# Kernel optimization log

Measured on AMD Instinct MI355X. Metric: run time of the kernel, lower is better.

Reference implementation:

```python
import jax, jax.numpy as jnp
import numpy as np

NQ, NK, H, DH = 1024, 512, 8, 64


def setup_inputs() -> dict:
    key = jax.random.key(0)
    ks = jax.random.split(key, 8)
    b, n, d, g = 4, 4096, 1024, 4
    di = H * DH  # 512
    s = lambda fan: 1.0 / np.sqrt(fan)
    return {
        "x": jax.random.normal(ks[0], (b, n, d), jnp.float32),
        "w_qr": jax.random.normal(ks[1], (g, d), jnp.float32) * s(d),
        "w_kvr": jax.random.normal(ks[2], (g, d), jnp.float32) * s(d),
        "w_q": jax.random.normal(ks[3], (g, di, d), jnp.float32) * s(d),
        "w_kv": jax.random.normal(ks[4], (g, 2 * di, d), jnp.float32) * s(d),
        "w_out": jax.random.normal(ks[5], (g, d, di), jnp.float32) * s(di),
        "null_kv": jax.random.normal(ks[6], (2, g, H, 1, DH), jnp.float32),
        "null_token": jax.random.normal(ks[7], (1, 1, d), jnp.float32),
    }


def reference(x, w_qr, w_kvr, w_q, w_kv, w_out, null_kv, null_token):
    b, n, d = x.shape
    g = w_qr.shape[0]
    bidx = jnp.arange(b)[:, None, None]
    # --- routing: per-expert token scores, top-k select (router reference) ---
    q_logits = jnp.einsum("bnd,gd->bgn", x, w_qr)
    q_top, q_idx = jax.lax.top_k(q_logits, NQ)            # [b,g,NQ]
    q_scores = jax.nn.sigmoid(q_top)[..., None]           # [b,g,NQ,1]
    queries = x[bidx, q_idx]                              # [b,g,NQ,d]
    kv_logits = jnp.einsum("bnd,gd->bgn", x, w_kvr)
    kv_top, kv_idx = jax.lax.top_k(kv_logits, NK)
    kv_scores = jax.nn.sigmoid(kv_top)[:, :, None, :, None]  # [b,g,1,NK,1]
    key_values = x[bidx, kv_idx]                          # [b,g,NK,d]
    # --- grouped attention (1x1 grouped convs == per-group matmuls) ---
    q = jnp.einsum("bgnd,ged->bgne", queries, w_q)
    kv = jnp.einsum("bgnd,ged->bgne", key_values, w_kv)
    k, v = jnp.split(kv, 2, axis=-1)
    heads = lambda t: t.reshape(b, g, -1, H, DH).transpose(0, 1, 3, 2, 4)  # b g h n dh
    q, k, v = heads(q), heads(k), heads(v)
    v = v * kv_scores                                     # values_scale
    nk = jnp.broadcast_to(null_kv[0][None], (b, g, H, 1, DH))
    nv = jnp.broadcast_to(null_kv[1][None], (b, g, H, 1, DH))
    k = jnp.concatenate([nk, k], axis=-2)
    v = jnp.concatenate([nv, v], axis=-2)
    attn = jax.nn.softmax(jnp.einsum("bghid,bghjd->bghij", q, k) * DH ** -0.5, axis=-1)
    o = jnp.einsum("bghij,bghjd->bghid", attn, v)
    o = o.transpose(0, 1, 3, 2, 4).reshape(b, g, NQ, H * DH)
    o = jnp.einsum("bgne,gde->bgnd", o, w_out)
    o = o * q_scores
    # --- scatter-add back with count normalization ---
    flat_idx = q_idx.reshape(b, g * NQ)
    flat_o = o.reshape(b, g * NQ, d)
    b2 = jnp.arange(b)[:, None]
    summed = jnp.zeros_like(x).at[b2, flat_idx].add(flat_o)
    counts = jnp.zeros((b, n), x.dtype).at[b2, flat_idx].add(1.0)[..., None]
    meaned = summed / jnp.clip(counts, 1e-5)
    return jnp.where(counts > 0, meaned, null_token)
```

## Files before the change

### kernel.cpp

```cpp
#include <hip/hip_runtime.h>
#include <math.h>

#define NB 4
#define SEQ 4096
#define DM 1024
#define NG 4
#define DI 512
#define NQS 1024
#define NKS 512
#define NHD 8
#define DHD 64
#define VTS 520

typedef unsigned int u32;
typedef unsigned short u16;
typedef __bf16 bf16x8 __attribute__((ext_vector_type(8)));
typedef float f32x4 __attribute__((ext_vector_type(4)));

__device__ __forceinline__ float bf2f(u16 u) { return __uint_as_float(((u32)u) << 16); }
__device__ __forceinline__ u16 f2bf(float f) {
  u32 u = __float_as_uint(f);
  u32 r = (u + 0x7FFFu + ((u >> 16) & 1u)) >> 16;
  return (u16)r;
}
__device__ __forceinline__ u16 f2bfh(float f) {
  union { __bf16 b; u16 u; } cv;
  cv.b = (__bf16)f;
  return cv.u;
}

__global__ __launch_bounds__(256) void router_kernel(
    const float* __restrict__ x, const float* __restrict__ wqr,
    const float* __restrict__ wkvr, float* __restrict__ qlog,
    float* __restrict__ kvlog, u16* __restrict__ xbf) {
  int tid = threadIdx.x;
  int base = blockIdx.x * 8 + (tid >> 6) * 2;
  int lane = tid & 63;
  int b = base >> 12, tok = base & 4095;
  const float4* xr0 = (const float4*)(x + ((size_t)(b * SEQ + tok)) * DM);
  const float4* xr1 = xr0 + 256;
  float4 xv0[4], xv1[4];
#pragma unroll
  for (int i = 0; i < 4; i++) {
    xv0[i] = xr0[i * 64 + lane];
    xv1[i] = xr1[i * 64 + lane];
  }
  ushort4* xrow0 = (ushort4*)(xbf + ((size_t)(b * SEQ + tok)) * DM);
  ushort4* xrow1 = xrow0 + 256;
#pragma unroll
  for (int i = 0; i < 4; i++) {
    ushort4 o0, o1;
    o0.x = f2bf(xv0[i].x); o0.y = f2bf(xv0[i].y);
    o0.z = f2bf(xv0[i].z); o0.w = f2bf(xv0[i].w);
    o1.x = f2bf(xv1[i].x); o1.y = f2bf(xv1[i].y);
    o1.z = f2bf(xv1[i].z); o1.w = f2bf(xv1[i].w);
    xrow0[i * 64 + lane] = o0;
    xrow1[i * 64 + lane] = o1;
  }
  float a0[8], a1[8];
#pragma unroll
  for (int r = 0; r < 8; r++) {
    const float4* wr =
        (const float4*)(r < 4 ? wqr + (r << 10) : wkvr + ((r - 4) << 10));
    float s0 = 0.f, s1 = 0.f;
#pragma unroll
    for (int i = 0; i < 4; i++) {
      float4 w4 = wr[i * 64 + lane];
      s0 += xv0[i].x * w4.x + xv0[i].y * w4.y + xv0[i].z * w4.z + xv0[i].w * w4.w;
      s1 += xv1[i].x * w4.x + xv1[i].y * w4.y + xv1[i].z * w4.z + xv1[i].w * w4.w;
    }
    a0[r] = s0; a1[r] = s1;
  }
#pragma unroll
  for (int r = 0; r < 8; r++) {
#pragma unroll
    for (int off = 32; off >= 1; off >>= 1) {
      a0[r] += __shfl_xor(a0[r], off);
      a1[r] += __shfl_xor(a1[r], off);
    }
    if (lane == 0) {
      if (r < 4) {
        qlog[((b << 2) | r) * SEQ + tok] = a0[r];
        qlog[((b << 2) | r) * SEQ + tok + 1] = a1[r];
      } else {
        kvlog[((b << 2) | (r - 4)) * SEQ + tok] = a0[r];
        kvlog[((b << 2) | (r - 4)) * SEQ + tok + 1] = a1[r];
      }
    }
  }
}

__global__ __launch_bounds__(256) void topk_kernel(
    const float* __restrict__ qlog, const float* __restrict__ kvlog,
    int* __restrict__ qidx, float* __restrict__ qscore,
    int* __restrict__ kvidx, float* __restrict__ kvscore,
    int* __restrict__ qpos, const float* __restrict__ wq,
    const float* __restrict__ wkv, const float* __restrict__ wout,
    u16* __restrict__ wqbf, u16* __restrict__ wkvbf, u16* __restrict__ woutbf) {
  int tid = threadIdx.x;
  if (blockIdx.x >= 32) {
    int cid = blockIdx.x - 32;
#pragma unroll
    for (int j = 0; j < 4; j++) {
      int idx = cid * 1024 + j * 256 + tid;
      const float* src; u16* dst; int off;
      if (idx < 524288)        { src = wq;   dst = wqbf;   off = idx; }
      else if (idx < 1572864)  { src = wkv;  dst = wkvbf;  off = idx - 524288; }
      else                     { src = wout; dst = woutbf; off = idx - 1572864; }
      float4 v = ((const float4*)src)[off];
      ushort4 o;
      o.x = f2bf(v.x); o.y = f2bf(v.y); o.z = f2bf(v.z); o.w = f2bf(v.w);
      ((ushort4*)dst)[off] = o;
    }
    return;
  }
  __shared__ u32 keys[4096];
  __shared__ int eqlist[2048];
  __shared__ int scnt[4];
  __shared__ int s_gt, s_eq;
  int which = blockIdx.x >> 4;
  int bg = blockIdx.x & 15;
  int K = (which == 0) ? NQS : NKS;
  const float* L = ((which == 0) ? qlog : kvlog) + bg * 4096;
  int* out_idx = ((which == 0) ? qidx : kvidx) + bg * K;
  float* out_score = ((which == 0) ? qscore : kvscore) + bg * K;
  int* qposb = qpos + bg * 4096;
  for (int e = tid; e < 4096; e += 256) {
    u32 u = __float_as_uint(L[e]);
    keys[e] = (u >> 31) ? ~u : (u | 0x80000000u);
  }
  if (which == 0)
    for (int e = tid; e < 4096; e += 256) qposb[e] = -1;
  if (tid == 0) { s_gt = 0; s_eq = 0; }
  __syncthreads();
  u32 prefix = 0;
  int remaining = K;
  for (int bit = 31; bit >= 0; --bit) {
    u32 want = prefix | (1u << bit);
    u32 mask = ~((1u << bit) - 1u);
    int c = 0;
    for (int e = tid; e < 4096; e += 256) c += ((keys[e] & mask) == want) ? 1 : 0;
#pragma unroll
    for (int off = 32; off >= 1; off >>= 1) c += __shfl_xor(c, off);
    if ((tid & 63) == 0) scnt[tid >> 6] = c;
    __syncthreads();
    int total = scnt[0] + scnt[1] + scnt[2] + scnt[3];
    if (total >= remaining) prefix = want;
    else remaining -= total;
    __syncthreads();
  }
  u32 T = prefix;
  for (int e = tid; e < 4096; e += 256) {
    u32 k = keys[e];
    if (k > T) {
      int pos = atomicAdd(&s_gt, 1);
      out_idx[pos] = e;
      u32 uo = (k >> 31) ? (k & 0x7FFFFFFFu) : ~k;
      float v = __uint_as_float(uo);
      out_score[pos] = 1.0f / (1.0f + __expf(-v));
      if (which == 0) qposb[e] = pos;
    } else if (k == T) {
      int p = atomicAdd(&s_eq, 1);
      if (p < 2048) eqlist[p] = e;
    }
  }
  __syncthreads();
  int gt = s_gt;
  int eq = min(s_eq, 2048);
  int need = K - gt;
  for (int i = tid; i < eq; i += 256) {
    int my = eqlist[i];
    int rank = 0;
    for (int j = 0; j < eq; j++) rank += (eqlist[j] < my) ? 1 : 0;
    if (rank < need) {
      int pos = gt + rank;
      out_idx[pos] = my;
      u32 k2 = keys[my];
      u32 uo = (k2 >> 31) ? (k2 & 0x7FFFFFFFu) : ~k2;
      float v = __uint_as_float(uo);
      out_score[pos] = 1.0f / (1.0f + __expf(-v));
      if (which == 0) qposb[my] = pos;
    }
  }
}

struct Ptr4 { const u16* p[4]; };

__device__ __forceinline__ void mfma_core(Ptr4 A, Ptr4 B, u16* Asm, u16* Bsm,
                                          int ktiles, int tid, f32x4 (&acc)[4][4]) {
  int w = tid >> 6, lane = tid & 63;
  int col = lane & 15, quad = lane >> 4;
  int wr = w >> 1, wc = w & 1;
  for (int kt = 0; kt < ktiles; kt++) {
#pragma unroll
    for (int r = 0; r < 4; r++) {
      char* ldsA = (char*)Asm + (r * 256 + w * 64) * 16;
      __builtin_amdgcn_global_load_lds(
          (const __attribute__((address_space(1))) void*)(A.p[r] + kt * 64),
          (__attribute__((address_space(3))) void*)ldsA, 16, 0, 0);
    }
#pragma unroll
    for (int r = 0; r < 4; r++) {
      char* ldsB = (char*)Bsm + (r * 256 + w * 64) * 16;
      __builtin_amdgcn_global_load_lds(
          (const __attribute__((address_space(1))) void*)(B.p[r] + kt * 64),
          (__attribute__((address_space(3))) void*)ldsB, 16, 0, 0);
    }
    __syncthreads();
#pragma unroll
    for (int k04 = 0; k04 < 8; k04 += 4) {
      bf16x8 af[4], bfr[4];
#pragma unroll
      for (int t = 0; t < 4; t++) {
        int rowa = wr * 64 + t * 16 + col;
        int sp = (quad + k04) ^ (col & 7);
        af[t] = *(const bf16x8*)((const char*)Asm + (rowa * 8 + sp) * 16);
        int rowb = wc * 64 + t * 16 + col;
        bfr[t] = *(const bf16x8*)((const char*)Bsm + (rowb * 8 + sp) * 16);
      }
#pragma unroll
      for (int t = 0; t < 4; t++)
#pragma unroll
        for (int u = 0; u < 4; u++)
          acc[t][u] = __builtin_amdgcn_mfma_f32_16x16x32_bf16(af[t], bfr[u], acc[t][u], 0, 0, 0);
    }
    __syncthreads();
  }
}

__global__ __launch_bounds__(256) void gemm_qkvproj(
    const u16* __restrict__ xbf, const int* __restrict__ qidx,
    const int* __restrict__ kvidx, const u16* __restrict__ wqbf,
    const u16* __restrict__ wkvbf, const float* __restrict__ kvscore,
    u16* __restrict__ qbuf, u16* __restrict__ kbuf, u16* __restrict__ vtbuf) {
  __shared__ __align__(16) u16 Asm[8192], Bsm[8192];
  __shared__ int ridx[128];
  int tid = threadIdx.x;
  int id = blockIdx.x;
  bool is_q = (id & 1) == 0;
  int sid = id >> 1;
  int bg = sid >> 5, r5 = sid & 31;
  int b = bg >> 2, g = bg & 3;
  int w = tid >> 6, lane = tid & 63;
  int col = lane & 15, quad = lane >> 4;
  int wr = w >> 1, wc = w & 1;

  if (is_q) {
    int col0 = (r5 & 3) * 128, row0 = (r5 >> 2) * 128;
    if (tid < 128) ridx[tid] = qidx[bg * NQS + row0 + tid];
    __syncthreads();
    Ptr4 A, B;
#pragma unroll
    for (int r = 0; r < 4; r++) {
      int G = r * 256 + tid;
      int row = G >> 3;
      int seg = (G & 7) ^ (row & 7);
      A.p[r] = xbf + ((size_t)b * SEQ + ridx[row]) * DM + seg * 8;
      B.p[r] = wqbf + ((size_t)g * DI + col0 + row) * DM + seg * 8;
    }
    f32x4 acc[4][4] = {};
    mfma_core(A, B, Asm, Bsm, DM / 64, tid, acc);
#pragma unroll
    for (int t = 0; t < 4; t++)
#pragma unroll
      for (int u = 0; u < 4; u++)
#pragma unroll
        for (int r = 0; r < 4; r++) {
          int rowg = row0 + wr * 64 + t * 16 + quad * 4 + r;
          int colg = col0 + wc * 64 + u * 16 + col;
          qbuf[((size_t)bg * NQS + rowg) * DI + colg] = f2bf(acc[t][u][r] * 0.125f);
        }
  } else {
    int col0 = (r5 & 7) * 128, row0 = (r5 >> 3) * 128;
    if (tid < 128) ridx[tid] = kvidx[bg * NKS + row0 + tid];
    __syncthreads();
    Ptr4 A, B;
#pragma unroll
    for (int r = 0; r < 4; r++) {
      int G = r * 256 + tid;
      int row = G >> 3;
      int seg = (G & 7) ^ (row & 7);
      A.p[r] = xbf + ((size_t)b * SEQ + ridx[row]) * DM + seg * 8;
      B.p[r] = wkvbf + ((size_t)g * (2 * DI) + col0 + row) * DM + seg * 8;
    }
    f32x4 acc[4][4] = {};
    mfma_core(A, B, Asm, Bsm, DM / 64, tid, acc);
    if (col0 < DI) {
#pragma unroll
      for (int t = 0; t < 4; t++)
#pragma unroll
        for (int u = 0; u < 4; u++)
#pragma unroll
          for (int r = 0; r < 4; r++) {
            int rowg = row0 + wr * 64 + t * 16 + quad * 4 + r;
            int colg = col0 + wc * 64 + u * 16 + col;
            kbuf[((size_t)bg * NKS + rowg) * DI + colg] = f2bf(acc[t][u][r]);
          }
    } else {
#pragma unroll
      for (int t = 0; t < 4; t++) {
        int base = row0 + wr * 64 + t * 16 + quad * 4;
        float sc0 = kvscore[bg * NKS + base + 0];
        float sc1 = kvscore[bg * NKS + base + 1];
        float sc2 = kvscore[bg * NKS + base + 2];
        float sc3 = kvscore[bg * NKS + base + 3];
#pragma unroll
        for (int u = 0; u < 4; u++) {
          int vc = col0 - DI + wc * 64 + u * 16 + col;
          int h = vc >> 6, d = vc & 63;
          u32 lo = (u32)f2bf(acc[t][u][0] * sc0) | ((u32)f2bf(acc[t][u][1] * sc1) << 16);
          u32 hi = (u32)f2bf(acc[t][u][2] * sc2) | ((u32)f2bf(acc[t][u][3] * sc3) << 16);
          *(uint2*)&vtbuf[(((size_t)bg * NHD + h) * DHD + d) * VTS + base] =
              make_uint2(lo, hi);
        }
      }
    }
  }
}

__global__ __launch_bounds__(256) void gemm_outproj(
    const u16* __restrict__ obuf, const u16* __restrict__ woutbf,
    const float* __restrict__ qscore, float* __restrict__ oproj_lo,
    float* __restrict__ oproj_hi) {
  int bg = blockIdx.z, g = bg & 3;
  int row0 = blockIdx.y * 128, col0 = blockIdx.x * 128;
  __shared__ __align__(16) u16 Asm[8192], Bsm[8192];
  int tid = threadIdx.x;
  Ptr4 A, B;
#pragma unroll
  for (int r = 0; r < 4; r++) {
    int G = r * 256 + tid;
    int row = G >> 3;
    int seg = (G & 7) ^ (row & 7);
    A.p[r] = obuf + ((size_t)bg * NQS + row0 + row) * DI + seg * 8;
    B.p[r] = woutbf + ((size_t)g * DM + col0 + row) * DI + seg * 8;
  }
  f32x4 acc[4][4] = {};
  mfma_core(A, B, Asm, Bsm, DI / 64, tid, acc);
  int w = tid >> 6, lane = tid & 63;
  int col = lane & 15, quad = lane >> 4;
  int wr = w >> 1, wc = w & 1;
  float* obase = (bg < 8 ? oproj_lo : oproj_hi) + (size_t)(bg & 7) * NQS * DM;
#pragma unroll
  for (int t = 0; t < 4; t++)
#pragma unroll
    for (int r = 0; r < 4; r++) {
      int rowg = row0 + wr * 64 + t * 16 + quad * 4 + r;
      float sc = qscore[bg * NQS + rowg];
      float* orow = obase + (size_t)rowg * DM;
#pragma unroll
      for (int u = 0; u < 4; u++) {
        int colg = col0 + wc * 64 + u * 16 + col;
        orow[colg] = acc[t][u][r] * sc;
      }
    }
}

__global__ __launch_bounds__(256) void finalize_gather(
    const float* __restrict__ oproj_lo, const float* __restrict__ oproj_hi,
    const int* __restrict__ qpos, const float* __restrict__ null_token,
    float* __restrict__ dout) {
  int blk = blockIdx.x;
  int b = blk >> 12;
  int tok = blk & 4095;
  int tid = threadIdx.x;
  const float* obase = (b < 2) ? oproj_lo : oproj_hi;
  int zoff = (b & 1) * 4;
  float4 acc = {0.f, 0.f, 0.f, 0.f};
  int cnt = 0;
#pragma unroll
  for (int g = 0; g < 4; g++) {
    int pos = qpos[(((b << 2) | g)) * 4096 + tok];
    if (pos >= 0) {
      const float4* row =
          (const float4*)(obase + ((size_t)(zoff + g) * NQS + pos) * DM);
      float4 v = row[tid];
      acc.x += v.x; acc.y += v.y; acc.z += v.z; acc.w += v.w;
      cnt++;
    }
  }
  float4* dst = (float4*)(dout + ((size_t)b * SEQ + tok) * DM) + tid;
  if (cnt > 0) {
    float inv = 1.0f / cnt;
    acc.x *= inv; acc.y *= inv; acc.z *= inv; acc.w *= inv;
    *dst = acc;
  } else {
    *dst = ((const float4*)null_token)[tid];
  }
}

__global__ __launch_bounds__(256, 4) void attn_mfma(
    const u16* __restrict__ qbuf, const u16* __restrict__ kbuf,
    const u16* __restrict__ vtbuf, const float* __restrict__ null_kv,
    u16* __restrict__ obuf) {
  int qt = blockIdx.x;
  int h = blockIdx.y;
  int bg = blockIdx.z;
  int g = bg & 3;
  int tid = threadIdx.x;
  int w = tid >> 6, lane = tid & 63;
  int col = lane & 15, quad = lane >> 4;

  __shared__ __align__(16) u16 Ks[64][72];
  __shared__ __align__(16) u16 Vts[64][72];
  __shared__ __align__(16) u16 Ps[4][32][72];

  int q0 = qt * 128 + w * 32;
  const u16* qp0 = qbuf + ((size_t)bg * NQS + q0 + col) * DI + h * DHD + quad * 8;
  bf16x8 qa[2][2];
  qa[0][0] = *(const bf16x8*)qp0;
  qa[0][1] = *(const bf16x8*)(qp0 + 32);
  qa[1][0] = *(const bf16x8*)(qp0 + 16 * DI);
  qa[1][1] = *(const bf16x8*)(qp0 + 16 * DI + 32);

  const float* kn = null_kv + ((size_t)(0 * NG + g) * NHD + h) * DHD;
  const float* vn = null_kv + ((size_t)(1 * NG + g) * NHD + h) * DHD;
  float m_run[2], l_lane[2];
  f32x4 oacc[2][4];
#pragma unroll
  for (int s = 0; s < 2; s++) {
    float sn = 0.f;
#pragma unroll
    for (int i = 0; i < 8; i++) {
      sn += (float)qa[s][0][i] * kn[quad * 8 + i];
      sn += (float)qa[s][1][i] * kn[32 + quad * 8 + i];
    }
    sn += __shfl_xor(sn, 16);
    sn += __shfl_xor(sn, 32);
    m_run[s] = sn;
    l_lane[s] = (quad == 0) ? 1.f : 0.f;
  }
#pragma unroll
  for (int t = 0; t < 4; t++) {
    float v = vn[t * 16 + col];
    f32x4 tmp = {v, v, v, v};
    oacc[0][t] = tmp;
    oacc[1][t] = tmp;
  }

  int sr = tid >> 2, ss = tid & 3;
  const u16* kptr = kbuf + ((size_t)bg * NKS + sr) * DI + h * DHD + ss * 16;
  const u16* vptr = vtbuf + (((size_t)bg * NHD + h) * DHD + sr) * VTS + ss * 16;
  uint4* kdst = (uint4*)&Ks[sr][ss * 16];
  uint4* vdst = (uint4*)&Vts[sr][ss * 16];
  uint4 ck0, ck1, cv0, cv1;
  { const uint4* p = (const uint4*)kptr; ck0 = p[0]; ck1 = p[1]; }
  { const uint4* p = (const uint4*)vptr; cv0 = p[0]; cv1 = p[1]; }

  for (int c = 0; c < 8; ++c) {
    kdst[0] = ck0; kdst[1] = ck1;
    vdst[0] = cv0; vdst[1] = cv1;
    if (c < 7) {
      const uint4* p = (const uint4*)(kptr + (size_t)(c + 1) * 64 * DI);
      ck0 = p[0]; ck1 = p[1];
      const uint4* q4 = (const uint4*)(vptr + (c + 1) * 64);
      cv0 = q4[0]; cv1 = q4[1];
    }
    __syncthreads();

    f32x4 sv[2][4];
#pragma unroll
    for (int t = 0; t < 4; t++) {
      bf16x8 kb0 = *(const bf16x8*)&Ks[t * 16 + col][quad * 8];
      bf16x8 kb1 = *(const bf16x8*)&Ks[t * 16 + col][quad * 8 + 32];
      f32x4 z = {0.f, 0.f, 0.f, 0.f};
      f32x4 s0 = __builtin_amdgcn_mfma_f32_16x16x32_bf16(kb0, qa[0][0], z, 0, 0, 0);
      sv[0][t] = __builtin_amdgcn_mfma_f32_16x16x32_bf16(kb1, qa[0][1], s0, 0, 0, 0);
      f32x4 s1 = __builtin_amdgcn_mfma_f32_16x16x32_bf16(kb0, qa[1][0], z, 0, 0, 0);
      sv[1][t] = __builtin_amdgcn_mfma_f32_16x16x32_bf16(kb1, qa[1][1], s1, 0, 0, 0);
    }

#pragma unroll
    for (int s = 0; s < 2; s++) {
      float pm = sv[s][0][0];
#pragma unroll
      for (int t = 0; t < 4; t++)
#pragma unroll
        for (int r = 0; r < 4; r++) pm = fmaxf(pm, sv[s][t][r]);
      pm = fmaxf(pm, __shfl_xor(pm, 16));
      pm = fmaxf(pm, __shfl_xor(pm, 32));
      if (!__all(pm <= m_run[s] + 8.0f)) {
        float mnew = fmaxf(m_run[s], pm);
        float alpha = __expf(m_run[s] - mnew);
        m_run[s] = mnew;
        l_lane[s] *= alpha;
#pragma unroll
        for (int r = 0; r < 4; r++) {
          float a_o = __shfl(alpha, quad * 4 + r);
#pragma unroll
          for (int t = 0; t < 4; t++) oacc[s][t][r] *= a_o;
        }
      }
      float rs = 0.f;
#pragma unroll
      for (int t = 0; t < 4; t++) {
        float p0 = __expf(sv[s][t][0] - m_run[s]);
        float p1 = __expf(sv[s][t][1] - m_run[s]);
        float p2 = __expf(sv[s][t][2] - m_run[s]);
        float p3 = __expf(sv[s][t][3] - m_run[s]);
        rs += (p0 + p1) + (p2 + p3);
        u32 lo = (u32)f2bfh(p0) | ((u32)f2bfh(p1) << 16);
        u32 hi = (u32)f2bfh(p2) | ((u32)f2bfh(p3) << 16);
        *(uint2*)&Ps[w][s * 16 + col][t * 16 + quad * 4] = make_uint2(lo, hi);
      }
      l_lane[s] += rs;
    }

#pragma unroll
    for (int s2 = 0; s2 < 2; s2++) {
      bf16x8 pa0 = *(const bf16x8*)&Ps[w][col][s2 * 32 + quad * 8];
      bf16x8 pa1 = *(const bf16x8*)&Ps[w][16 + col][s2 * 32 + quad * 8];
#pragma unroll
      for (int t = 0; t < 4; t++) {
        bf16x8 vb = *(const bf16x8*)&Vts[t * 16 + col][s2 * 32 + quad * 8];
        oacc[0][t] = __builtin_amdgcn_mfma_f32_16x16x32_bf16(pa0, vb, oacc[0][t], 0, 0, 0);
        oacc[1][t] = __builtin_amdgcn_mfma_f32_16x16x32_bf16(pa1, vb, oacc[1][t], 0, 0, 0);
      }
    }
    __syncthreads();
  }

#pragma unroll
  for (int s = 0; s < 2; s++) {
    float l = l_lane[s];
    l += __shfl_xor(l, 16);
    l += __shfl_xor(l, 32);
    float inv = 1.0f / l;
#pragma unroll
    for (int r = 0; r < 4; r++) {
      float ir = __shfl(inv, quad * 4 + r);
#pragma unroll
      for (int t = 0; t < 4; t++) {
        obuf[((size_t)bg * NQS + q0 + s * 16 + quad * 4 + r) * DI + h * DHD +
             t * 16 + col] = f2bfh(oacc[s][t][r] * ir);
      }
    }
  }
}

extern "C" void kernel_launch(void* const* d_in, const int* in_sizes, int n_in,
                              void* d_out, int out_size, void* d_ws, size_t ws_size,
                              hipStream_t stream) {
  const float* x = (const float*)d_in[0];
  const float* wqr = (const float*)d_in[1];
  const float* wkvr = (const float*)d_in[2];
  const float* wq = (const float*)d_in[3];
  const float* wkv = (const float*)d_in[4];
  const float* wout = (const float*)d_in[5];
  const float* nullkv = (const float*)d_in[6];
  const float* nulltok = (const float*)d_in[7];
  float* out = (float*)d_out;
  char* ws = (char*)d_ws;
  float* qlog = (float*)(ws + 0);
  float* kvlog = (float*)(ws + 262144);
  int* qidx = (int*)(ws + 524288);
  int* kvidx = (int*)(ws + 589824);
  float* qscore = (float*)(ws + 622592);
  float* kvscore = (float*)(ws + 688128);
  u16* qbuf = (u16*)(ws + 786432);
  u16* kbuf = (u16*)(ws + 17563648);
  u16* vtbuf = (u16*)(ws + 25952256);
  u16* obuf = (u16*)(ws + 34476032);
  u16* xbf = (u16*)(ws + 51253248);
  u16* wqbf = (u16*)(ws + 84807680);
  u16* wkvbf = (u16*)(ws + 89001984);
  u16* woutbf = (u16*)(ws + 97390592);
  int* qpos = (int*)(ws + 0);
  float* oproj_lo = (float*)(ws + 786432);
  float* oproj_hi = (float*)(ws + 51253248);

  router_kernel<<<2048, 256, 0, stream>>>(x, wqr, wkvr, qlog, kvlog, xbf);
  topk_kernel<<<2080, 256, 0, stream>>>(qlog, kvlog, qidx, qscore, kvidx,
                                        kvscore, qpos, wq, wkv, wout, wqbf,
                                        wkvbf, woutbf);
  gemm_qkvproj<<<1024, 256, 0, stream>>>(xbf, qidx, kvidx, wqbf, wkvbf, kvscore,
                                         qbuf, kbuf, vtbuf);
  attn_mfma<<<dim3(8, 8, 16), 256, 0, stream>>>(qbuf, kbuf, vtbuf, nullkv, obuf);
  gemm_outproj<<<dim3(8, 8, 16), 256, 0, stream>>>(obuf, woutbf, qscore,
                                                   oproj_lo, oproj_hi);
  finalize_gather<<<16384, 256, 0, stream>>>(oproj_lo, oproj_hi, qpos, nulltok,
                                             out);
}
```

Measured before the change: 316.7 us.

## Store out-projection in bf16, shorten top-k radix passes, remap attention grid

The out-projection intermediate is now written as bf16 instead of fp32, and finalize_gather reads it back as bf16. This halves the bytes written and re-read between those two kernels, at the cost of rounding before the per-token averaging. The top-k radix select stops after 20 bits, which cuts the number of count passes. Remaining ties are then ranked by full key and index, so the selection stays exact as long as the tie list fits its buffer. The attention launch becomes a 1D grid whose block decode puts heads and batch-groups innermost, which changes the block scheduling order.

```diff
diff --git a/kernel.cpp b/kernel.cpp
--- a/kernel.cpp
+++ b/kernel.cpp
@@ -135,7 +135,7 @@
   __syncthreads();
   u32 prefix = 0;
   int remaining = K;
-  for (int bit = 31; bit >= 0; --bit) {
+  for (int bit = 31; bit >= 12; --bit) {
     u32 want = prefix | (1u << bit);
     u32 mask = ~((1u << bit) - 1u);
     int c = 0;
@@ -152,14 +152,15 @@
   u32 T = prefix;
   for (int e = tid; e < 4096; e += 256) {
     u32 k = keys[e];
-    if (k > T) {
+    u32 k20 = k & 0xFFFFF000u;
+    if (k20 > T) {
       int pos = atomicAdd(&s_gt, 1);
       out_idx[pos] = e;
       u32 uo = (k >> 31) ? (k & 0x7FFFFFFFu) : ~k;
       float v = __uint_as_float(uo);
       out_score[pos] = 1.0f / (1.0f + __expf(-v));
       if (which == 0) qposb[e] = pos;
-    } else if (k == T) {
+    } else if (k20 == T) {
       int p = atomicAdd(&s_eq, 1);
       if (p < 2048) eqlist[p] = e;
     }
@@ -170,13 +171,16 @@
   int need = K - gt;
   for (int i = tid; i < eq; i += 256) {
     int my = eqlist[i];
+    u32 myk = keys[my];
     int rank = 0;
-    for (int j = 0; j < eq; j++) rank += (eqlist[j] < my) ? 1 : 0;
+    for (int j = 0; j < eq; j++) {
+      u32 kj = keys[eqlist[j]];
+      rank += (kj > myk || (kj == myk && eqlist[j] < my)) ? 1 : 0;
+    }
     if (rank < need) {
       int pos = gt + rank;
       out_idx[pos] = my;
-      u32 k2 = keys[my];
-      u32 uo = (k2 >> 31) ? (k2 & 0x7FFFFFFFu) : ~k2;
+      u32 uo = (myk >> 31) ? (myk & 0x7FFFFFFFu) : ~myk;
       float v = __uint_as_float(uo);
       out_score[pos] = 1.0f / (1.0f + __expf(-v));
       if (which == 0) qposb[my] = pos;
@@ -320,8 +324,8 @@
 
 __global__ __launch_bounds__(256) void gemm_outproj(
     const u16* __restrict__ obuf, const u16* __restrict__ woutbf,
-    const float* __restrict__ qscore, float* __restrict__ oproj_lo,
-    float* __restrict__ oproj_hi) {
+    const float* __restrict__ qscore, u16* __restrict__ oproj_lo,
+    u16* __restrict__ oproj_hi) {
   int bg = blockIdx.z, g = bg & 3;
   int row0 = blockIdx.y * 128, col0 = blockIdx.x * 128;
   __shared__ __align__(16) u16 Asm[8192], Bsm[8192];
@@ -340,31 +344,31 @@
   int w = tid >> 6, lane = tid & 63;
   int col = lane & 15, quad = lane >> 4;
   int wr = w >> 1, wc = w & 1;
-  float* obase = (bg < 8 ? oproj_lo : oproj_hi) + (size_t)(bg & 7) * NQS * DM;
+  u16* obase = (bg < 8 ? oproj_lo : oproj_hi) + (size_t)(bg & 7) * NQS * DM;
 #pragma unroll
   for (int t = 0; t < 4; t++)
 #pragma unroll
     for (int r = 0; r < 4; r++) {
       int rowg = row0 + wr * 64 + t * 16 + quad * 4 + r;
       float sc = qscore[bg * NQS + rowg];
-      float* orow = obase + (size_t)rowg * DM;
+      u16* orow = obase + (size_t)rowg * DM;
 #pragma unroll
       for (int u = 0; u < 4; u++) {
         int colg = col0 + wc * 64 + u * 16 + col;
-        orow[colg] = acc[t][u][r] * sc;
+        orow[colg] = f2bfh(acc[t][u][r] * sc);
       }
     }
 }
 
 __global__ __launch_bounds__(256) void finalize_gather(
-    const float* __restrict__ oproj_lo, const float* __restrict__ oproj_hi,
+    const u16* __restrict__ oproj_lo, const u16* __restrict__ oproj_hi,
     const int* __restrict__ qpos, const float* __restrict__ null_token,
     float* __restrict__ dout) {
   int blk = blockIdx.x;
   int b = blk >> 12;
   int tok = blk & 4095;
   int tid = threadIdx.x;
-  const float* obase = (b < 2) ? oproj_lo : oproj_hi;
+  const u16* obase = (b < 2) ? oproj_lo : oproj_hi;
   int zoff = (b & 1) * 4;
   float4 acc = {0.f, 0.f, 0.f, 0.f};
   int cnt = 0;
@@ -372,10 +376,13 @@
   for (int g = 0; g < 4; g++) {
     int pos = qpos[(((b << 2) | g)) * 4096 + tok];
     if (pos >= 0) {
-      const float4* row =
-          (const float4*)(obase + ((size_t)(zoff + g) * NQS + pos) * DM);
-      float4 v = row[tid];
-      acc.x += v.x; acc.y += v.y; acc.z += v.z; acc.w += v.w;
+      const uint2* row =
+          (const uint2*)(obase + ((size_t)(zoff + g) * NQS + pos) * DM);
+      uint2 v = row[tid];
+      acc.x += bf2f((u16)(v.x & 0xFFFF));
+      acc.y += bf2f((u16)(v.x >> 16));
+      acc.z += bf2f((u16)(v.y & 0xFFFF));
+      acc.w += bf2f((u16)(v.y >> 16));
       cnt++;
     }
   }
@@ -393,9 +400,10 @@
     const u16* __restrict__ qbuf, const u16* __restrict__ kbuf,
     const u16* __restrict__ vtbuf, const float* __restrict__ null_kv,
     u16* __restrict__ obuf) {
-  int qt = blockIdx.x;
-  int h = blockIdx.y;
-  int bg = blockIdx.z;
+  int id = blockIdx.x;
+  int qt = id >> 7;
+  int h = id & 7;
+  int bg = (id >> 3) & 15;
   int g = bg & 3;
   int tid = threadIdx.x;
   int w = tid >> 6, lane = tid & 63;
@@ -566,8 +574,8 @@
   u16* wkvbf = (u16*)(ws + 89001984);
   u16* woutbf = (u16*)(ws + 97390592);
   int* qpos = (int*)(ws + 0);
-  float* oproj_lo = (float*)(ws + 786432);
-  float* oproj_hi = (float*)(ws + 51253248);
+  u16* oproj_lo = (u16*)(ws + 786432);
+  u16* oproj_hi = (u16*)(ws + 51253248);
 
   router_kernel<<<2048, 256, 0, stream>>>(x, wqr, wkvr, qlog, kvlog, xbf);
   topk_kernel<<<2080, 256, 0, stream>>>(qlog, kvlog, qidx, qscore, kvidx,
@@ -575,7 +583,7 @@
                                         wkvbf, woutbf);
   gemm_qkvproj<<<1024, 256, 0, stream>>>(xbf, qidx, kvidx, wqbf, wkvbf, kvscore,
                                          qbuf, kbuf, vtbuf);
-  attn_mfma<<<dim3(8, 8, 16), 256, 0, stream>>>(qbuf, kbuf, vtbuf, nullkv, obuf);
+  attn_mfma<<<1024, 256, 0, stream>>>(qbuf, kbuf, vtbuf, nullkv, obuf);
   gemm_outproj<<<dim3(8, 8, 16), 256, 0, stream>>>(obuf, woutbf, qscore,
                                                    oproj_lo, oproj_hi);
   finalize_gather<<<16384, 256, 0, stream>>>(oproj_lo, oproj_hi, qpos, nulltok,
```

New measurement: 301.1 us. 1.05x faster.
